# Performance work log

Measured on AMD Instinct MI355X. Metric: run time of the kernel, lower is better.

Reference implementation:

```python
import jax, jax.numpy as jnp
import numpy as np

B, T, DFEAT = 2, 2048, 1024
DIM, DEPTH, H, DH = 512, 2, 8, 64
INNER = H * DH  # 512
MLP = 512
RED1, RED2 = DIM // 16, DIM // 32  # 32, 16
EPS = 1e-5


def _ln(x, g, b):
    m = jnp.mean(x, axis=-1, keepdims=True)
    v = jnp.mean((x - m) ** 2, axis=-1, keepdims=True)
    return (x - m) * jax.lax.rsqrt(v + EPS) * g + b


def _bn_eval(x, g, b, rm, rv):
    # x: [B, C, T]; eval-mode BatchNorm1d with running stats
    return (x - rm[:, None]) * jax.lax.rsqrt(rv[:, None] + EPS) * g[:, None] + b[:, None]


def setup_inputs() -> dict:
    key = jax.random.key(0)
    ks = iter(jax.random.split(key, 64))
    rn = lambda shape, s=0.02: (jax.random.normal(next(ks), shape, dtype=jnp.float32) * s)
    inp = {}
    inp['x'] = jax.random.normal(next(ks), (B, T, DFEAT), dtype=jnp.float32)
    # Temporal embedding conv (k=3, pad=1), OIW layout
    inp['emb_w'] = rn((DIM, DFEAT, 3))
    inp['emb_b'] = jnp.zeros((DIM,), jnp.float32)
    # Transformer: stacked per-layer params [DEPTH, ...]
    inp['ln1_g'] = jnp.ones((DEPTH, DIM), jnp.float32)
    inp['ln1_b'] = jnp.zeros((DEPTH, DIM), jnp.float32)
    inp['wqkvt'] = rn((DEPTH, DIM, 4 * INNER))
    inp['wout'] = rn((DEPTH, 2 * INNER, DIM))
    inp['bout'] = jnp.zeros((DEPTH, DIM), jnp.float32)
    inp['ln2_g'] = jnp.ones((DEPTH, DIM), jnp.float32)
    inp['ln2_b'] = jnp.zeros((DEPTH, DIM), jnp.float32)
    inp['w1'] = rn((DEPTH, DIM, MLP))
    inp['b1'] = jnp.zeros((DEPTH, MLP), jnp.float32)
    inp['w2'] = rn((DEPTH, MLP, DIM))
    inp['b2'] = jnp.zeros((DEPTH, DIM), jnp.float32)
    # NormalHead (k=1 convs -> pointwise), eval-mode BN params
    inp['h1_w'] = rn((RED1, DIM)); inp['h1_b'] = jnp.zeros((RED1,), jnp.float32)
    inp['bn1_g'] = jnp.ones((RED1,), jnp.float32); inp['bn1_b'] = jnp.zeros((RED1,), jnp.float32)
    inp['bn1_m'] = jnp.zeros((RED1,), jnp.float32); inp['bn1_v'] = jnp.ones((RED1,), jnp.float32)
    inp['h2_w'] = rn((RED2, RED1)); inp['h2_b'] = jnp.zeros((RED2,), jnp.float32)
    inp['bn2_g'] = jnp.ones((RED2,), jnp.float32); inp['bn2_b'] = jnp.zeros((RED2,), jnp.float32)
    inp['bn2_m'] = jnp.zeros((RED2,), jnp.float32); inp['bn2_v'] = jnp.ones((RED2,), jnp.float32)
    inp['h3_w'] = rn((1, RED2)); inp['h3_b'] = jnp.zeros((1,), jnp.float32)
    return inp


def _attention(x, wqkvt, wout, bout, attn2):
    b, n, d = x.shape
    qkvt = x @ wqkvt  # [b, n, 4*INNER]
    q, k, v, t = jnp.split(qkvt, 4, axis=-1)
    sp = lambda z: z.reshape(b, n, H, DH).transpose(0, 2, 1, 3)  # b h n d
    q, k, v, t = sp(q), sp(k), sp(v), sp(t)
    scale = DH ** -0.5
    dots = jnp.einsum('bhid,bhjd->bhij', q, k) * scale
    attn1 = jax.nn.softmax(dots, axis=-1)
    out1 = jnp.einsum('bhij,bhjd->bhid', attn1, v)
    out2 = jnp.einsum('ij,bhjd->bhid', attn2, t)
    out = jnp.concatenate([out1, out2], axis=-1)  # b h n 2*DH
    out = out.transpose(0, 2, 1, 3).reshape(b, n, 2 * INNER)
    return out @ wout + bout


def _forward(x, emb_w, emb_b, ln1_g, ln1_b, wqkvt, wout, bout, ln2_g, ln2_b,
             w1, b1, w2, b2, h1_w, h1_b, bn1_g, bn1_b, bn1_m, bn1_v,
             h2_w, h2_b, bn2_g, bn2_b, bn2_m, bn2_v, h3_w, h3_b):
    # Temporal embedding: Conv1d(k=3,pad=1) + ReLU over time axis
    xc = x.transpose(0, 2, 1)  # [B, DFEAT, T]
    emb = jax.lax.conv_general_dilated(xc, emb_w, (1,), 'SAME',
                                       dimension_numbers=('NCH', 'OIH', 'NCH'))
    emb = jax.nn.relu(emb + emb_b[None, :, None])
    h = emb.transpose(0, 2, 1)  # [B, T, DIM]
    # fixed temporal-decay attention matrix (batch/head independent)
    idx = jnp.arange(T, dtype=jnp.float32)
    tg = jnp.abs(idx[None, :] - idx[:, None])
    a2 = jnp.exp(-tg / jnp.float32(np.e))
    attn2 = a2 / a2.sum(-1)  # torch broadcast: divide along last axis
    for l in range(DEPTH):
        h = h + _attention(_ln(h, ln1_g[l], ln1_b[l]), wqkvt[l], wout[l], bout[l], attn2)
        z = _ln(h, ln2_g[l], ln2_b[l])
        z = jax.nn.gelu(z @ w1[l] + b1[l], approximate=False) @ w2[l] + b2[l]
        h = h + z
    # NormalHead on [B, DIM, T] with k=1 convs
    y = h.transpose(0, 2, 1)
    f1 = jnp.einsum('oc,bct->bot', h1_w, y) + h1_b[None, :, None]
    f2 = jnp.einsum('oc,bct->bot', h2_w, jax.nn.relu(_bn_eval(f1, bn1_g, bn1_b, bn1_m, bn1_v))) + h2_b[None, :, None]
    f3 = jnp.einsum('oc,bct->bot', h3_w, jax.nn.relu(_bn_eval(f2, bn2_g, bn2_b, bn2_m, bn2_v))) + h3_b[None, :, None]
    scores = jax.nn.sigmoid(f3)[:, 0, :]  # [B, T]
    return scores


def reference(x, emb_w, emb_b, ln1_g, ln1_b, wqkvt, wout, bout, ln2_g, ln2_b,
              w1, b1, w2, b2, h1_w, h1_b, bn1_g, bn1_b, bn1_m, bn1_v,
              h2_w, h2_b, bn2_g, bn2_b, bn2_m, bn2_v, h3_w, h3_b):
    return _forward(x, emb_w, emb_b, ln1_g, ln1_b, wqkvt, wout, bout, ln2_g, ln2_b,
                    w1, b1, w2, b2, h1_w, h1_b, bn1_g, bn1_b, bn1_m, bn1_v,
                    h2_w, h2_b, bn2_g, bn2_b, bn2_m, bn2_v, h3_w, h3_b)
```

## Files before the change

kernel.cpp:

```cpp
#include <hip/hip_runtime.h>
#include <hip/hip_bf16.h>
#include <math.h>

#define TN 2048
#define BN 2
#define DF 1024
#define DM 512
#define NHD 8
#define DHD 64
#define INV_E 0.36787944117144233f
#define R_DECAY 0.69220062755534635f

typedef float f32x4 __attribute__((ext_vector_type(4)));
typedef __bf16 bf16x8 __attribute__((ext_vector_type(8)));
typedef unsigned short ushort8 __attribute__((ext_vector_type(8)));
typedef unsigned short ushort4v __attribute__((ext_vector_type(4)));
typedef unsigned short u16;

__device__ inline u16 f2bf(float f) {
    __hip_bfloat16 b = __float2bfloat16(f);
    return __builtin_bit_cast(u16, b);
}
__device__ inline float bf2f(u16 u) {
    unsigned int x = ((unsigned int)u) << 16;
    return __builtin_bit_cast(float, x);
}
__device__ inline bf16x8 ldbf8(const u16* p) {
    return __builtin_bit_cast(bf16x8, *(const ushort8*)p);
}

struct WtrAll {
    const float* src[8];
    u16* dst[8];
    int K[8], N[8], start[8], mask[8], shift[8];
};

__global__ __launch_bounds__(256) void wtr_all_kernel(WtrAll a) {
    __shared__ u16 tile[64][67];
    int bid = blockIdx.x;
    int w = 0;
#pragma unroll
    for (int i = 1; i < 8; ++i)
        if (bid >= a.start[i]) w = i;
    const float* src = a.src[w];
    u16* dst = a.dst[w];
    int K = a.K[w], N = a.N[w];
    int t0 = bid - a.start[w];
    int bx = t0 & a.mask[w], by = t0 >> a.shift[w];
    int t = threadIdx.x;
    int tr = t >> 4, tc = (t & 15) * 4;
#pragma unroll
    for (int rr = 0; rr < 4; ++rr) {
        int kl = tr + rr * 16;
        float4 v = *(const float4*)&src[(size_t)(by * 64 + kl) * N + bx * 64 + tc];
        tile[kl][tc + 0] = f2bf(v.x);
        tile[kl][tc + 1] = f2bf(v.y);
        tile[kl][tc + 2] = f2bf(v.z);
        tile[kl][tc + 3] = f2bf(v.w);
    }
    __syncthreads();
#pragma unroll
    for (int rr = 0; rr < 4; ++rr) {
        int nl = tr + rr * 16;
        ushort4v o;
#pragma unroll
        for (int q = 0; q < 4; ++q) o[q] = tile[tc + q][nl];
        *(ushort4v*)&dst[(size_t)(bx * 64 + nl) * K + by * 64 + tc] = o;
    }
}

__global__ __launch_bounds__(256) void emb_tr_kernel(const float* __restrict__ w,
                                                     u16* __restrict__ dst) {
    int idx = blockIdx.x * 256 + threadIdx.x;
    if (idx >= DM * 3 * DF) return;
    int o = idx / (3 * DF);
    int rem = idx - o * 3 * DF;
    int tap = rem / DF, i = rem - tap * DF;
    dst[idx] = f2bf(w[(size_t)o * 3 * DF + i * 3 + tap]);
}

__global__ __launch_bounds__(256) void sinv_kernel(float* __restrict__ sinv) {
    int j = blockIdx.x * 256 + threadIdx.x;
    if (j >= TN) return;
    float r = __expf(-INV_E);
    float inv1mr = 1.f / (1.f - r);
    float a = (1.f - __expf(-(float)(j + 1) * INV_E)) * inv1mr;
    float b = (r - __expf(-(float)(TN - j) * INV_E)) * inv1mr;
    sinv[j] = 1.f / (a + b);
}

__global__ __launch_bounds__(256) void xshift_kernel(const float* __restrict__ x,
                                                     u16* __restrict__ xs) {
    int idx = blockIdx.x * 256 + threadIdx.x;
    if (idx >= BN * TN * 3 * DF / 8) return;
    int row = idx / (3 * DF / 8);
    int kc = (idx - row * (3 * DF / 8)) * 8;
    int b = row >> 11, t = row & (TN - 1);
    int tap = kc / DF, i = kc - tap * DF;
    int tt = t + tap - 1;
    ushort8 o;
    if (tt < 0 || tt >= TN) {
        for (int q = 0; q < 8; ++q) o[q] = 0;
    } else {
        const float4* p = (const float4*)&x[((size_t)b * TN + tt) * DF + i];
        float4 v0 = p[0], v1 = p[1];
        o[0] = f2bf(v0.x); o[1] = f2bf(v0.y); o[2] = f2bf(v0.z); o[3] = f2bf(v0.w);
        o[4] = f2bf(v1.x); o[5] = f2bf(v1.y); o[6] = f2bf(v1.z); o[7] = f2bf(v1.w);
    }
    *(ushort8*)&xs[(size_t)row * 3 * DF + kc] = o;
}

template <int MODE, int BM, int BNT>
__global__ __launch_bounds__(256) void gemm2(const u16* __restrict__ A,
                                             const u16* __restrict__ Bt,
                                             const float* __restrict__ bias,
                                             const float* resid, void* outp,
                                             int M, int N, int K) {
    constexpr int MR = BM / 32, NR = BNT / 32;
    constexpr int PA = BM / 64, PB = BNT / 64;
    __shared__ __align__(16) u16 As[2][BM][72];
    __shared__ __align__(16) u16 Bs[2][BNT][72];
    int tid = threadIdx.x;
    int lane = tid & 63, wid = tid >> 6;
    int m0 = blockIdx.y * BM, n0 = blockIdx.x * BNT;
    int wm = (wid >> 1) * (BM / 2), wn = (wid & 1) * (BNT / 2);
    int fr = lane & 15, kq = (lane >> 4) * 8;
    int srow = tid >> 2, scol = (tid & 3) * 16;
    f32x4 acc[MR][NR] = {};
    const u16* Ap = A + (size_t)(m0 + srow) * K + scol;
    const u16* Bp = Bt + (size_t)(n0 + srow) * K + scol;
    ushort8 ra[PA][2], rb[PB][2];
#pragma unroll
    for (int p = 0; p < PA; ++p) {
        ra[p][0] = *(const ushort8*)(Ap + (size_t)p * 64 * K);
        ra[p][1] = *(const ushort8*)(Ap + (size_t)p * 64 * K + 8);
    }
#pragma unroll
    for (int p = 0; p < PB; ++p) {
        rb[p][0] = *(const ushort8*)(Bp + (size_t)p * 64 * K);
        rb[p][1] = *(const ushort8*)(Bp + (size_t)p * 64 * K + 8);
    }
    int nt = K >> 6;
    int pb = 0;
    for (int t = 0; t < nt; ++t) {
#pragma unroll
        for (int p = 0; p < PA; ++p) {
            *(ushort8*)&As[pb][srow + p * 64][scol] = ra[p][0];
            *(ushort8*)&As[pb][srow + p * 64][scol + 8] = ra[p][1];
        }
#pragma unroll
        for (int p = 0; p < PB; ++p) {
            *(ushort8*)&Bs[pb][srow + p * 64][scol] = rb[p][0];
            *(ushort8*)&Bs[pb][srow + p * 64][scol + 8] = rb[p][1];
        }
        __syncthreads();
        if (t + 1 < nt) {
            int ko = (t + 1) << 6;
#pragma unroll
            for (int p = 0; p < PA; ++p) {
                ra[p][0] = *(const ushort8*)(Ap + (size_t)p * 64 * K + ko);
                ra[p][1] = *(const ushort8*)(Ap + (size_t)p * 64 * K + ko + 8);
            }
#pragma unroll
            for (int p = 0; p < PB; ++p) {
                rb[p][0] = *(const ushort8*)(Bp + (size_t)p * 64 * K + ko);
                rb[p][1] = *(const ushort8*)(Bp + (size_t)p * 64 * K + ko + 8);
            }
        }
#pragma unroll
        for (int kc = 0; kc < 2; ++kc) {
            bf16x8 af[MR], bf[NR];
#pragma unroll
            for (int a = 0; a < MR; ++a) af[a] = ldbf8(&As[pb][wm + a * 16 + fr][kc * 32 + kq]);
#pragma unroll
            for (int b = 0; b < NR; ++b) bf[b] = ldbf8(&Bs[pb][wn + b * 16 + fr][kc * 32 + kq]);
#pragma unroll
            for (int a = 0; a < MR; ++a)
#pragma unroll
                for (int b = 0; b < NR; ++b)
                    acc[a][b] = __builtin_amdgcn_mfma_f32_16x16x32_bf16(af[a], bf[b], acc[a][b], 0, 0, 0);
        }
        pb ^= 1;
    }
    int rq = (lane >> 4) * 4;
#pragma unroll
    for (int a = 0; a < MR; ++a)
#pragma unroll
        for (int b = 0; b < NR; ++b) {
            int col = n0 + wn + b * 16 + fr;
            float bv = (MODE & 1) ? bias[col] : 0.f;
#pragma unroll
            for (int r = 0; r < 4; ++r) {
                int row = m0 + wm + a * 16 + rq + r;
                float v = acc[a][b][r] + bv;
                if (MODE & 2) v = fmaxf(v, 0.f);
                if (MODE & 4) v = 0.5f * v * (1.f + erff(v * 0.7071067811865476f));
                if (MODE & 8) v += resid[(size_t)row * N + col];
                if (MODE & 16) ((float*)outp)[(size_t)row * N + col] = v;
                else           ((u16*)outp)[(size_t)row * N + col] = f2bf(v);
            }
        }
}

__global__ __launch_bounds__(256) void ln_kernel(const float* __restrict__ h,
                                                 const float* __restrict__ g,
                                                 const float* __restrict__ bta,
                                                 u16* __restrict__ outp) {
    int lane = threadIdx.x & 63, wid = threadIdx.x >> 6;
    int row = blockIdx.x * 4 + wid;
    const float4* xp = (const float4*)(h + (size_t)row * DM + lane * 8);
    float4 v0 = xp[0], v1 = xp[1];
    float v[8] = {v0.x, v0.y, v0.z, v0.w, v1.x, v1.y, v1.z, v1.w};
    float s = 0.f;
#pragma unroll
    for (int i = 0; i < 8; ++i) s += v[i];
    for (int sft = 1; sft < 64; sft <<= 1) s += __shfl_xor(s, sft, 64);
    float mean = s * (1.f / DM);
    float q = 0.f;
#pragma unroll
    for (int i = 0; i < 8; ++i) { float d = v[i] - mean; q += d * d; }
    for (int sft = 1; sft < 64; sft <<= 1) q += __shfl_xor(q, sft, 64);
    float rs = rsqrtf(q * (1.f / DM) + 1e-5f);
    ushort8 o;
#pragma unroll
    for (int i = 0; i < 8; ++i) {
        float y = (v[i] - mean) * rs * g[lane * 8 + i] + bta[lane * 8 + i];
        o[i] = f2bf(y);
    }
    *(ushort8*)&outp[(size_t)row * DM + lane * 8] = o;
}

__global__ __launch_bounds__(256) void attn_split(const u16* __restrict__ qkvt,
                                                  u16* __restrict__ po,
                                                  float* __restrict__ pl) {
    __shared__ __align__(16) u16 Ks[64][72];
    __shared__ __align__(16) u16 Vs[64][72];
    __shared__ __align__(16) u16 Ps[4][16][72];
    int tid = threadIdx.x;
    int lane = tid & 63, wid = tid >> 6;
    int bid = blockIdx.x;
    int cc = bid & 3, qb = (bid >> 2) & 31, hh = (bid >> 7) & 7, b = bid >> 10;
    int fr = lane & 15, kq = (lane >> 4) * 8, rq = (lane >> 4) * 4;

    int qrow = qb * 64 + wid * 16 + fr;
    bf16x8 aq[2];
#pragma unroll
    for (int kc = 0; kc < 2; ++kc) {
        bf16x8 t = ldbf8(&qkvt[((size_t)(b * TN + qrow)) * 2048 + hh * 64 + kc * 32 + kq]);
        bf16x8 sc;
#pragma unroll
        for (int i = 0; i < 8; ++i) sc[i] = (__bf16)(0.125f * (float)t[i]);
        aq[kc] = sc;
    }

    f32x4 o[4];
#pragma unroll
    for (int cb = 0; cb < 4; ++cb) o[cb] = f32x4{0.f, 0.f, 0.f, 0.f};
    float rsum[4] = {0.f, 0.f, 0.f, 0.f};

    int srow = tid >> 3, scol = (tid & 7) * 8;
    int vxw = ((scol >> 3) & 7) << 3;
    int pxw = rq << 1;
    for (int kb = 0; kb < 8; ++kb) {
        int j0 = cc * 512 + kb * 64;
#pragma unroll
        for (int half = 0; half < 2; ++half) {
            int jr = srow + half * 32;
            size_t rbase = ((size_t)(b * TN + j0 + jr)) * 2048;
            *(ushort8*)&Ks[jr][scol] = *(const ushort8*)&qkvt[rbase + 512 + hh * 64 + scol];
            ushort8 vv = *(const ushort8*)&qkvt[rbase + 1024 + hh * 64 + scol];
            int jc = jr ^ vxw;
#pragma unroll
            for (int i = 0; i < 8; ++i) Vs[scol + i][jc] = vv[i];
        }
        __syncthreads();
#pragma unroll
        for (int jb = 0; jb < 4; ++jb) {
            f32x4 sa = f32x4{0.f, 0.f, 0.f, 0.f};
#pragma unroll
            for (int kc = 0; kc < 2; ++kc) {
                bf16x8 bk = ldbf8(&Ks[jb * 16 + fr][kc * 32 + kq]);
                sa = __builtin_amdgcn_mfma_f32_16x16x32_bf16(aq[kc], bk, sa, 0, 0, 0);
            }
#pragma unroll
            for (int r = 0; r < 4; ++r) {
                float p = __expf(sa[r]);
                rsum[r] += p;
                Ps[wid][rq + r][(jb * 16 + fr) ^ pxw] = f2bf(p);
            }
        }
        bf16x8 pa[2];
#pragma unroll
        for (int kc = 0; kc < 2; ++kc)
            pa[kc] = ldbf8(&Ps[wid][fr][(kc * 32 + kq) ^ ((fr & 12) << 1)]);
#pragma unroll
        for (int cb = 0; cb < 4; ++cb)
#pragma unroll
            for (int kc = 0; kc < 2; ++kc) {
                int vrow = cb * 16 + fr;
                bf16x8 bv = ldbf8(&Vs[vrow][(kc * 32 + kq) ^ (((vrow >> 3) & 7) << 3)]);
                o[cb] = __builtin_amdgcn_mfma_f32_16x16x32_bf16(pa[kc], bv, o[cb], 0, 0, 0);
            }
        __syncthreads();
    }
#pragma unroll
    for (int r = 0; r < 4; ++r)
        for (int sft = 1; sft < 16; sft <<= 1) rsum[r] += __shfl_xor(rsum[r], sft, 64);
#pragma unroll
    for (int r = 0; r < 4; ++r) {
        int grow = (b * NHD + hh) * TN + qb * 64 + wid * 16 + rq + r;
        size_t pidx = (size_t)grow * 4 + cc;
#pragma unroll
        for (int cb = 0; cb < 4; ++cb)
            po[pidx * 64 + cb * 16 + fr] = f2bf(o[cb][r]);
        if (fr == 0) pl[pidx] = rsum[r];
    }
}

__global__ __launch_bounds__(256) void attn_combine(const u16* __restrict__ po,
                                                    const float* __restrict__ pl,
                                                    u16* __restrict__ attcat) {
    int lane = threadIdx.x & 63, wid = threadIdx.x >> 6;
    int R = blockIdx.x * 4 + wid;
    float l = 0.f, ov = 0.f;
#pragma unroll
    for (int cc = 0; cc < 4; ++cc) {
        l += pl[R * 4 + cc];
        ov += bf2f(po[((size_t)R * 4 + cc) * 64 + lane]);
    }
    int bh = R >> 11, q = R & (TN - 1);
    int b = bh >> 3, hh = bh & 7;
    attcat[((size_t)(b * TN + q)) * 1024 + hh * 128 + lane] = f2bf(ov / l);
}

#define BCH 32
__global__ __launch_bounds__(256) void band_scan_kernel(const u16* __restrict__ qkvt,
                                                        const float* __restrict__ sinv,
                                                        u16* __restrict__ attcat) {
    int tid = blockIdx.x * 256 + threadIdx.x;
    int c = tid & 511;
    int rest = tid >> 9;
    int chunk = rest & 63;
    int b = rest >> 6;
    int i0 = chunk * BCH;
    const float r = R_DECAY;
    const u16* tcol = qkvt + 1536 + c;
    float regs[BCH];
    float st = 0.f;
    for (int j = i0 - 32; j < i0; ++j) {
        if (j >= 0) st = r * st + sinv[j] * bf2f(tcol[(size_t)(b * TN + j) * 2048]);
    }
#pragma unroll
    for (int k = 0; k < BCH; ++k) {
        int j = i0 + k;
        st = r * st + sinv[j] * bf2f(tcol[(size_t)(b * TN + j) * 2048]);
        regs[k] = st;
    }
    st = 0.f;
    for (int j = i0 + BCH + 31; j >= i0 + BCH; --j) {
        if (j < TN) st = r * st + sinv[j] * bf2f(tcol[(size_t)(b * TN + j) * 2048]);
    }
#pragma unroll
    for (int k = BCH - 1; k >= 0; --k) {
        int j = i0 + k;
        regs[k] += r * st;
        st = r * st + sinv[j] * bf2f(tcol[(size_t)(b * TN + j) * 2048]);
    }
    int outcol = (c >> 6) * 128 + 64 + (c & 63);
#pragma unroll
    for (int k = 0; k < BCH; ++k)
        attcat[((size_t)(b * TN + i0 + k)) * 1024 + outcol] = f2bf(regs[k]);
}

__global__ __launch_bounds__(256) void head_kernel(
    const float* __restrict__ h, const float* __restrict__ h1w, const float* __restrict__ h1b,
    const float* __restrict__ bn1g, const float* __restrict__ bn1b,
    const float* __restrict__ bn1m, const float* __restrict__ bn1v,
    const float* __restrict__ h2w, const float* __restrict__ h2b,
    const float* __restrict__ bn2g, const float* __restrict__ bn2b,
    const float* __restrict__ bn2m, const float* __restrict__ bn2v,
    const float* __restrict__ h3w, const float* __restrict__ h3b,
    float* __restrict__ outp) {
    int lane = threadIdx.x & 63, wid = threadIdx.x >> 6;
    int idx = blockIdx.x * 4 + wid;
    const float4* xp = (const float4*)(h + (size_t)idx * DM + lane * 8);
    float4 v0 = xp[0], v1 = xp[1];
    float v[8] = {v0.x, v0.y, v0.z, v0.w, v1.x, v1.y, v1.z, v1.w};
    float a1[32];
#pragma unroll
    for (int o = 0; o < 32; ++o) {
        const float4* wp = (const float4*)(h1w + (size_t)o * DM + lane * 8);
        float4 w0 = wp[0], w1v = wp[1];
        a1[o] = w0.x * v[0] + w0.y * v[1] + w0.z * v[2] + w0.w * v[3] +
                w1v.x * v[4] + w1v.y * v[5] + w1v.z * v[6] + w1v.w * v[7];
    }
    for (int sft = 1; sft < 64; sft <<= 1) {
#pragma unroll
        for (int o = 0; o < 32; ++o) a1[o] += __shfl_xor(a1[o], sft, 64);
    }
    float r1[32];
#pragma unroll
    for (int o = 0; o < 32; ++o) {
        float f = a1[o] + h1b[o];
        f = (f - bn1m[o]) * rsqrtf(bn1v[o] + 1e-5f) * bn1g[o] + bn1b[o];
        r1[o] = fmaxf(f, 0.f);
    }
    float r2[16];
#pragma unroll
    for (int p = 0; p < 16; ++p) {
        float s = h2b[p];
#pragma unroll
        for (int o = 0; o < 32; ++o) s = fmaf(h2w[p * 32 + o], r1[o], s);
        s = (s - bn2m[p]) * rsqrtf(bn2v[p] + 1e-5f) * bn2g[p] + bn2b[p];
        r2[p] = fmaxf(s, 0.f);
    }
    float f3 = h3b[0];
#pragma unroll
    for (int p = 0; p < 16; ++p) f3 = fmaf(h3w[p], r2[p], f3);
    if (lane == 0) outp[idx] = 1.f / (1.f + __expf(-f3));
}

extern "C" void kernel_launch(void* const* d_in, const int* in_sizes, int n_in,
                              void* d_out, int out_size, void* d_ws, size_t ws_size,
                              hipStream_t stream) {
    const float* x     = (const float*)d_in[0];
    const float* emb_w = (const float*)d_in[1];
    const float* emb_b = (const float*)d_in[2];
    const float* ln1_g = (const float*)d_in[3];
    const float* ln1_b = (const float*)d_in[4];
    const float* wqkvt = (const float*)d_in[5];
    const float* wout  = (const float*)d_in[6];
    const float* bout  = (const float*)d_in[7];
    const float* ln2_g = (const float*)d_in[8];
    const float* ln2_b = (const float*)d_in[9];
    const float* w1    = (const float*)d_in[10];
    const float* b1    = (const float*)d_in[11];
    const float* w2    = (const float*)d_in[12];
    const float* b2    = (const float*)d_in[13];
    const float* h1w   = (const float*)d_in[14];
    const float* h1b   = (const float*)d_in[15];
    const float* bn1g  = (const float*)d_in[16];
    const float* bn1b  = (const float*)d_in[17];
    const float* bn1m  = (const float*)d_in[18];
    const float* bn1v  = (const float*)d_in[19];
    const float* h2w   = (const float*)d_in[20];
    const float* h2b   = (const float*)d_in[21];
    const float* bn2g  = (const float*)d_in[22];
    const float* bn2b  = (const float*)d_in[23];
    const float* bn2m  = (const float*)d_in[24];
    const float* bn2v  = (const float*)d_in[25];
    const float* h3w   = (const float*)d_in[26];
    const float* h3b   = (const float*)d_in[27];
    float* outp = (float*)d_out;

    char* ws = (char*)d_ws;
    size_t off = 0;
    auto take = [&](size_t bytes) {
        char* p = ws + off;
        off = (off + bytes + 255) & ~(size_t)255;
        return p;
    };
    const size_t MB = 1024 * 1024;
    float* h    = (float*)take((size_t)BN * TN * DM * 4);
    char* Pr    = take(18 * MB);
    u16* attcat = (u16*)take((size_t)BN * TN * 1024 * 2);
    float* sinv = (float*)take(TN * 4);
    u16* embwt  = (u16*)take((size_t)DM * 3 * DF * 2);
    u16* wqt    = (u16*)take((size_t)2 * 2048 * DM * 2);
    u16* woutt  = (u16*)take((size_t)2 * DM * 1024 * 2);
    u16* w1t    = (u16*)take((size_t)2 * DM * DM * 2);
    u16* w2t    = (u16*)take((size_t)2 * DM * DM * 2);
    u16* U      = (u16*)take((size_t)BN * TN * 3 * DF * 2);
    u16* xs = U;
    u16* qkvtb = U;
    u16* xln  = (u16*)Pr;
    u16* z1   = (u16*)(Pr + 4 * MB);
    float* pl = (float*)Pr;
    u16* po   = (u16*)(Pr + 1 * MB);
    (void)ws_size; (void)in_sizes; (void)n_in; (void)out_size;

    emb_tr_kernel<<<dim3(DM * 3 * DF / 256), dim3(256), 0, stream>>>(emb_w, embwt);
    {
        WtrAll a;
        int cur = 0;
        for (int l = 0; l < 2; ++l) {
            int e = l * 4;
            a.src[e + 0] = wqkvt + (size_t)l * 512 * 2048; a.dst[e + 0] = wqt + (size_t)l * 2048 * 512;
            a.K[e + 0] = 512;  a.N[e + 0] = 2048; a.start[e + 0] = cur; a.mask[e + 0] = 31; a.shift[e + 0] = 5; cur += 256;
            a.src[e + 1] = wout + (size_t)l * 1024 * 512;  a.dst[e + 1] = woutt + (size_t)l * 512 * 1024;
            a.K[e + 1] = 1024; a.N[e + 1] = 512;  a.start[e + 1] = cur; a.mask[e + 1] = 7;  a.shift[e + 1] = 3; cur += 128;
            a.src[e + 2] = w1 + (size_t)l * 512 * 512;     a.dst[e + 2] = w1t + (size_t)l * 512 * 512;
            a.K[e + 2] = 512;  a.N[e + 2] = 512;  a.start[e + 2] = cur; a.mask[e + 2] = 7;  a.shift[e + 2] = 3; cur += 64;
            a.src[e + 3] = w2 + (size_t)l * 512 * 512;     a.dst[e + 3] = w2t + (size_t)l * 512 * 512;
            a.K[e + 3] = 512;  a.N[e + 3] = 512;  a.start[e + 3] = cur; a.mask[e + 3] = 7;  a.shift[e + 3] = 3; cur += 64;
        }
        wtr_all_kernel<<<dim3(cur), dim3(256), 0, stream>>>(a);
    }
    sinv_kernel<<<dim3(TN / 256), dim3(256), 0, stream>>>(sinv);
    xshift_kernel<<<dim3(BN * TN * 3 * DF / 8 / 256), dim3(256), 0, stream>>>(x, xs);

    gemm2<19, 64, 64><<<dim3(DM / 64, BN * TN / 64), dim3(256), 0, stream>>>(
        xs, embwt, emb_b, nullptr, h, BN * TN, DM, 3 * DF);

    for (int l = 0; l < 2; ++l) {
        ln_kernel<<<dim3(BN * TN / 4), dim3(256), 0, stream>>>(h, ln1_g + l * DM, ln1_b + l * DM, xln);
        gemm2<0, 128, 128><<<dim3(2048 / 128, BN * TN / 128), dim3(256), 0, stream>>>(
            xln, wqt + (size_t)l * 2048 * 512, nullptr, nullptr, qkvtb, BN * TN, 2048, DM);
        attn_split<<<dim3(BN * NHD * (TN / 64) * 4), dim3(256), 0, stream>>>(qkvtb, po, pl);
        attn_combine<<<dim3(BN * NHD * TN / 4), dim3(256), 0, stream>>>(po, pl, attcat);
        band_scan_kernel<<<dim3(BN * 512 * (TN / BCH) / 256), dim3(256), 0, stream>>>(qkvtb, sinv, attcat);
        gemm2<25, 64, 64><<<dim3(DM / 64, BN * TN / 64), dim3(256), 0, stream>>>(
            attcat, woutt + (size_t)l * 512 * 1024, bout + l * DM, h, h, BN * TN, DM, 1024);
        ln_kernel<<<dim3(BN * TN / 4), dim3(256), 0, stream>>>(h, ln2_g + l * DM, ln2_b + l * DM, xln);
        gemm2<5, 64, 64><<<dim3(DM / 64, BN * TN / 64), dim3(256), 0, stream>>>(
            xln, w1t + (size_t)l * 512 * 512, b1 + l * DM, nullptr, z1, BN * TN, DM, DM);
        gemm2<25, 64, 64><<<dim3(DM / 64, BN * TN / 64), dim3(256), 0, stream>>>(
            z1, w2t + (size_t)l * 512 * 512, b2 + l * DM, h, h, BN * TN, DM, DM);
    }
    head_kernel<<<dim3(BN * TN / 4), dim3(256), 0, stream>>>(
        h, h1w, h1b, bn1g, bn1b, bn1m, bn1v, h2w, h2b, bn2g, bn2b, bn2m, bn2v, h3w, h3b, outp);
}
```

Before: 341.1 us.

## Double-buffer K/V tiles and pass P via bpermute instead of LDS in attention

The split attention kernel now prefetches the next K/V tile into registers while computing on the current one, with double-buffered shared memory, which removes one barrier per iteration. The QK^T MFMA operands are swapped so scores come out transposed. P is then repacked to bf16 and moved into A-operand layout with ds_bpermute, which drops the Ps shared buffer and its store/load round trip. The row-sum reduction is simplified to match, and a launch-bounds occupancy hint is added. This adds register pressure and extra permute instructions in exchange for fewer barriers and better overlap of loads with compute.

```diff
diff --git a/kernel.cpp b/kernel.cpp
--- a/kernel.cpp
+++ b/kernel.cpp
@@ -15,7 +15,9 @@
 typedef __bf16 bf16x8 __attribute__((ext_vector_type(8)));
 typedef unsigned short ushort8 __attribute__((ext_vector_type(8)));
 typedef unsigned short ushort4v __attribute__((ext_vector_type(4)));
+typedef unsigned int u32x4 __attribute__((ext_vector_type(4)));
 typedef unsigned short u16;
+typedef unsigned int u32;
 
 __device__ inline u16 f2bf(float f) {
     __hip_bfloat16 b = __float2bfloat16(f);
@@ -230,12 +232,11 @@
     *(ushort8*)&outp[(size_t)row * DM + lane * 8] = o;
 }
 
-__global__ __launch_bounds__(256) void attn_split(const u16* __restrict__ qkvt,
-                                                  u16* __restrict__ po,
-                                                  float* __restrict__ pl) {
-    __shared__ __align__(16) u16 Ks[64][72];
-    __shared__ __align__(16) u16 Vs[64][72];
-    __shared__ __align__(16) u16 Ps[4][16][72];
+__global__ __launch_bounds__(256, 4) void attn_split(const u16* __restrict__ qkvt,
+                                                     u16* __restrict__ po,
+                                                     float* __restrict__ pl) {
+    __shared__ __align__(16) u16 Ks[2][64][72];
+    __shared__ __align__(16) u16 Vs[2][64][72];
     int tid = threadIdx.x;
     int lane = tid & 63, wid = tid >> 6;
     int bid = blockIdx.x;
@@ -256,56 +257,106 @@
     f32x4 o[4];
 #pragma unroll
     for (int cb = 0; cb < 4; ++cb) o[cb] = f32x4{0.f, 0.f, 0.f, 0.f};
-    float rsum[4] = {0.f, 0.f, 0.f, 0.f};
+    float rsum = 0.f;
 
     int srow = tid >> 3, scol = (tid & 7) * 8;
     int vxw = ((scol >> 3) & 7) << 3;
-    int pxw = rq << 1;
-    for (int kb = 0; kb < 8; ++kb) {
-        int j0 = cc * 512 + kb * 64;
-#pragma unroll
-        for (int half = 0; half < 2; ++half) {
-            int jr = srow + half * 32;
-            size_t rbase = ((size_t)(b * TN + j0 + jr)) * 2048;
-            *(ushort8*)&Ks[jr][scol] = *(const ushort8*)&qkvt[rbase + 512 + hh * 64 + scol];
-            ushort8 vv = *(const ushort8*)&qkvt[rbase + 1024 + hh * 64 + scol];
-            int jc = jr ^ vxw;
-#pragma unroll
-            for (int i = 0; i < 8; ++i) Vs[scol + i][jc] = vv[i];
+    int i01 = (fr + ((lane & 16) << 1)) << 2;
+    int i23 = i01 + 64;
+    bool hi2 = (lane & 32) != 0;
+
+    ushort8 rk[2], rv[2];
+#pragma unroll
+    for (int half = 0; half < 2; ++half) {
+        int jr = srow + half * 32;
+        size_t rbase = ((size_t)(b * TN + cc * 512 + jr)) * 2048;
+        rk[half] = *(const ushort8*)&qkvt[rbase + 512 + hh * 64 + scol];
+        rv[half] = *(const ushort8*)&qkvt[rbase + 1024 + hh * 64 + scol];
+    }
+    int cur = 0;
+#pragma unroll
+    for (int half = 0; half < 2; ++half) {
+        int jr = srow + half * 32;
+        *(ushort8*)&Ks[0][jr][scol] = rk[half];
+        int jc = jr ^ vxw;
+#pragma unroll
+        for (int i = 0; i < 8; ++i) Vs[0][scol + i][jc] = rv[half][i];
+    }
+
+    for (int t = 0; t < 8; ++t) {
+        if (t < 7) {
+            int j0 = cc * 512 + (t + 1) * 64;
+#pragma unroll
+            for (int half = 0; half < 2; ++half) {
+                int jr = srow + half * 32;
+                size_t rbase = ((size_t)(b * TN + j0 + jr)) * 2048;
+                rk[half] = *(const ushort8*)&qkvt[rbase + 512 + hh * 64 + scol];
+                rv[half] = *(const ushort8*)&qkvt[rbase + 1024 + hh * 64 + scol];
+            }
         }
         __syncthreads();
+        float p[4][4];
 #pragma unroll
         for (int jb = 0; jb < 4; ++jb) {
             f32x4 sa = f32x4{0.f, 0.f, 0.f, 0.f};
 #pragma unroll
             for (int kc = 0; kc < 2; ++kc) {
-                bf16x8 bk = ldbf8(&Ks[jb * 16 + fr][kc * 32 + kq]);
-                sa = __builtin_amdgcn_mfma_f32_16x16x32_bf16(aq[kc], bk, sa, 0, 0, 0);
+                bf16x8 bk = ldbf8(&Ks[cur][jb * 16 + fr][kc * 32 + kq]);
+                sa = __builtin_amdgcn_mfma_f32_16x16x32_bf16(bk, aq[kc], sa, 0, 0, 0);
             }
 #pragma unroll
             for (int r = 0; r < 4; ++r) {
-                float p = __expf(sa[r]);
-                rsum[r] += p;
-                Ps[wid][rq + r][(jb * 16 + fr) ^ pxw] = f2bf(p);
-            }
-        }
+                p[jb][r] = __expf(sa[r]);
+                rsum += p[jb][r];
+            }
+        }
+        u32 pkr[4][2];
+#pragma unroll
+        for (int jb = 0; jb < 4; ++jb)
+#pragma unroll
+            for (int rp = 0; rp < 2; ++rp)
+                pkr[jb][rp] = ((u32)f2bf(p[jb][2 * rp + 1]) << 16) | (u32)f2bf(p[jb][2 * rp]);
         bf16x8 pa[2];
 #pragma unroll
-        for (int kc = 0; kc < 2; ++kc)
-            pa[kc] = ldbf8(&Ps[wid][fr][(kc * 32 + kq) ^ ((fr & 12) << 1)]);
+        for (int kc = 0; kc < 2; ++kc) {
+            u32 a0 = (u32)__builtin_amdgcn_ds_bpermute(i01, (int)pkr[kc * 2][0]);
+            u32 b0 = (u32)__builtin_amdgcn_ds_bpermute(i01, (int)pkr[kc * 2 + 1][0]);
+            u32 a1 = (u32)__builtin_amdgcn_ds_bpermute(i01, (int)pkr[kc * 2][1]);
+            u32 b1 = (u32)__builtin_amdgcn_ds_bpermute(i01, (int)pkr[kc * 2 + 1][1]);
+            u32 a2 = (u32)__builtin_amdgcn_ds_bpermute(i23, (int)pkr[kc * 2][0]);
+            u32 b2 = (u32)__builtin_amdgcn_ds_bpermute(i23, (int)pkr[kc * 2 + 1][0]);
+            u32 a3 = (u32)__builtin_amdgcn_ds_bpermute(i23, (int)pkr[kc * 2][1]);
+            u32 b3 = (u32)__builtin_amdgcn_ds_bpermute(i23, (int)pkr[kc * 2 + 1][1]);
+            u32x4 w;
+            w[0] = hi2 ? b0 : a0;
+            w[1] = hi2 ? b1 : a1;
+            w[2] = hi2 ? b2 : a2;
+            w[3] = hi2 ? b3 : a3;
+            pa[kc] = __builtin_bit_cast(bf16x8, w);
+        }
 #pragma unroll
         for (int cb = 0; cb < 4; ++cb)
 #pragma unroll
             for (int kc = 0; kc < 2; ++kc) {
                 int vrow = cb * 16 + fr;
-                bf16x8 bv = ldbf8(&Vs[vrow][(kc * 32 + kq) ^ (((vrow >> 3) & 7) << 3)]);
+                bf16x8 bv = ldbf8(&Vs[cur][vrow][(kc * 32 + kq) ^ (((vrow >> 3) & 7) << 3)]);
                 o[cb] = __builtin_amdgcn_mfma_f32_16x16x32_bf16(pa[kc], bv, o[cb], 0, 0, 0);
             }
-        __syncthreads();
-    }
-#pragma unroll
-    for (int r = 0; r < 4; ++r)
-        for (int sft = 1; sft < 16; sft <<= 1) rsum[r] += __shfl_xor(rsum[r], sft, 64);
+        if (t < 7) {
+            int nb = cur ^ 1;
+#pragma unroll
+            for (int half = 0; half < 2; ++half) {
+                int jr = srow + half * 32;
+                *(ushort8*)&Ks[nb][jr][scol] = rk[half];
+                int jc = jr ^ vxw;
+#pragma unroll
+                for (int i = 0; i < 8; ++i) Vs[nb][scol + i][jc] = rv[half][i];
+            }
+            cur = nb;
+        }
+    }
+    rsum += __shfl_xor(rsum, 16, 64);
+    rsum += __shfl_xor(rsum, 32, 64);
 #pragma unroll
     for (int r = 0; r < 4; ++r) {
         int grow = (b * NHD + hh) * TN + qb * 64 + wid * 16 + rq + r;
@@ -313,7 +364,10 @@
 #pragma unroll
         for (int cb = 0; cb < 4; ++cb)
             po[pidx * 64 + cb * 16 + fr] = f2bf(o[cb][r]);
-        if (fr == 0) pl[pidx] = rsum[r];
+    }
+    if (lane < 16) {
+        int grow = (b * NHD + hh) * TN + qb * 64 + wid * 16 + fr;
+        pl[(size_t)grow * 4 + cc] = rsum;
     }
 }
 
```

Result: no change. 338.1 us (-0.9%).
